# Optimization experiments

Hardware: AMD Instinct MI355X
Metric: run time of the kernel (lower is better)

## Reference

```python
import jax, jax.numpy as jnp
import numpy as np

B, N, F_IN, T = 8, 325, 32, 24
H, C = 4, 32  # num_heads, out_channels
K = 3         # k_neighbors


def _build_graph(seed=0):
    rng = np.random.default_rng(seed)
    dist = rng.uniform(0.1, 1.0, size=(N, N)).astype(np.float32)
    np.fill_diagonal(dist, 0.0)
    # per-row: k nearest among strictly-positive distances
    masked = np.where(dist > 0, dist, np.inf)
    idx = np.argsort(masked, axis=1)[:, :K]           # (N, K)
    rows = np.arange(N)[:, None]
    nd = dist[rows, idx]                              # (N, K)
    w = 1.0 / (nd + 1e-6)
    w = w / (w.sum(axis=1, keepdims=True) + 1e-6)
    adj_mask = np.zeros((N, N), np.float32)
    init_w = np.zeros((N, N), np.float32)
    adj_mask[rows, idx] = 1.0
    init_w[rows, idx] = w
    return adj_mask, init_w


def setup_inputs() -> dict:
    key = jax.random.key(0)
    k1, k2, k3, k4 = jax.random.split(key, 4)
    adj_mask, init_w = _build_graph()
    x = jax.random.normal(k1, (B, N, F_IN, T), dtype=jnp.float32)
    W_w = jax.random.normal(k2, (H * C, F_IN), dtype=jnp.float32) * (1.0 / np.sqrt(F_IN))
    W_b = jnp.zeros((H * C,), dtype=jnp.float32)
    attn_w = jax.random.normal(k3, (H, 2 * C), dtype=jnp.float32) * (1.0 / np.sqrt(2 * C))
    return {
        "x": x,
        "W_w": W_w,
        "W_b": W_b,
        "attn_w": attn_w,
        "initial_weights": jnp.asarray(init_w),
        "initial_weights_base": jnp.asarray(init_w),
        "adj_mask": jnp.asarray(adj_mask),
    }


def _constrain(w, base, adj_mask):
    w = jnp.clip(w, base * 0.5, base * 1.5)
    w = jnp.maximum(w, 0.0)
    s = jnp.sum(w * adj_mask, axis=1, keepdims=True)
    s = s + (s == 0).astype(w.dtype) * 1e-6
    return w * adj_mask / s


def reference(x, W_w, W_b, attn_w, initial_weights, initial_weights_base, adj_mask):
    b, n, f_in, t = x.shape
    xp = jnp.transpose(x, (0, 3, 1, 2))                    # (B,T,N,F)
    Wh = (xp @ W_w.T + W_b).reshape(b, t, n, H, C)         # (B,T,N,H,C)
    w = _constrain(initial_weights, initial_weights_base, adj_mask)
    a1, a2 = attn_w[:, :C], attn_w[:, C:]
    # attn(cat[Wh_i, Wh_j]) == Wh_i.a1 + Wh_j.a2 (no bias)
    f1 = jnp.einsum('btnhc,hc->btnh', Wh, a1)
    f2 = jnp.einsum('btnhc,hc->btnh', Wh, a2)
    e = f1[:, :, :, None, :] + f2[:, :, None, :, :]        # (B,T,N,N,H)
    score = jax.nn.leaky_relu(e, negative_slope=0.2)
    score = score * adj_mask[None, None, :, :, None] + w[None, None, :, :, None]
    attention = jax.nn.softmax(score, axis=3)              # softmax over j (includes zeroed non-edges, as in torch)
    out = jnp.einsum('btijh,btjhc->btihc', attention, Wh).reshape(b, t, n, H * C)
    return jnp.transpose(out, (0, 2, 3, 1))                # (B,N,H*C,T)
```

## Files before the change

kernel.cpp:

```cpp
#include <hip/hip_runtime.h>
#include <math.h>

#define Bq 8
#define Nq 325
#define F_INq 32
#define Tq 24
#define HCq 128
#define KMAX 4

__global__ __launch_bounds__(192) void prep_kernel(
    const float* __restrict__ iw, const float* __restrict__ ib,
    const float* __restrict__ adj, const float* __restrict__ Ww,
    const float* __restrict__ Wb, const float* __restrict__ attnw,
    const float* __restrict__ x,
    int* __restrict__ nbr_cnt, int* __restrict__ nbr_idx, float* __restrict__ nbr_w,
    float* __restrict__ Wx, float* __restrict__ WxT, float* __restrict__ Wp,
    float* __restrict__ bx, float* __restrict__ xp) {
  int blk = blockIdx.x;
  int tid = threadIdx.x;
  if (blk < Nq) {
    if (tid >= 64) return;
    int lane = tid;
    int i = blk;
    const float* iwr = iw + (size_t)i * Nq;
    const float* ibr = ib + (size_t)i * Nq;
    const float* ar  = adj + (size_t)i * Nq;
    float wa_c[6], a_c[6];
    float sum = 0.f;
    #pragma unroll
    for (int c = 0; c < 6; ++c) {
      int j = c * 64 + lane;
      float wa = 0.f, a = 0.f;
      if (j < Nq) {
        float basev = ibr[j];
        float w = iwr[j];
        w = fminf(fmaxf(w, basev * 0.5f), basev * 1.5f);
        w = fmaxf(w, 0.f);
        a = ar[j];
        wa = w * a;
      }
      wa_c[c] = wa; a_c[c] = a;
      sum += wa;
    }
    #pragma unroll
    for (int off = 32; off >= 1; off >>= 1) sum += __shfl_xor(sum, off, 64);
    if (sum == 0.f) sum = 1e-6f;
    float inv = 1.f / sum;
    unsigned long long below = (1ull << lane) - 1ull;
    int base = 0;
    #pragma unroll
    for (int c = 0; c < 6; ++c) {
      int j = c * 64 + lane;
      bool pred = (j < Nq) && (a_c[c] != 0.f);
      unsigned long long m = __ballot(pred);
      int rank = base + __popcll(m & below);
      if (pred && rank < KMAX) {
        nbr_idx[i * KMAX + rank] = j;
        nbr_w[i * KMAX + rank]   = wa_c[c] * inv;
      }
      base += __popcll(m);
    }
    if (lane == 0) {
      int cnt = base < KMAX ? base : KMAX;
      for (int k = cnt; k < KMAX; ++k) { nbr_idx[i * KMAX + k] = 0; nbr_w[i * KMAX + k] = 0.f; }
      nbr_cnt[i] = cnt;
    }
    return;
  }
  if (blk == Nq) {
    for (int o = tid; o < HCq * F_INq; o += 192) Wx[o] = Ww[o];
    for (int o = tid; o < F_INq * HCq; o += 192) {
      int f = o >> 7, r = o & 127;
      WxT[o] = Ww[r * F_INq + f];
    }
    for (int o = tid; o < 8 * F_INq; o += 192) {
      int p = o >> 5, f = o & 31;
      int h = p & 3, c0 = (p < 4) ? 0 : 32;
      float v = 0.f;
      for (int c = 0; c < 32; ++c)
        v += Ww[(h * 32 + c) * F_INq + f] * attnw[h * 64 + c0 + c];
      Wp[o] = v;
    }
    for (int r = tid; r < 136; r += 192) {
      float v;
      if (r < HCq) {
        v = Wb[r];
      } else {
        int h = (r - HCq) & 3, c0 = (r < 132) ? 0 : 32;
        v = 0.f;
        for (int c = 0; c < 32; ++c) v += Wb[h * 32 + c] * attnw[h * 64 + c0 + c];
      }
      bx[r] = v;
    }
    return;
  }
  {
    int pblk = blk - (Nq + 1);
    int b = pblk / 13, c = pblk - b * 13;
    const float4* src = (const float4*)x + ((size_t)b * Nq + c * 25) * 192;
    float4 a = {0.f, 0.f, 0.f, 0.f};
    #pragma unroll 5
    for (int n = 0; n < 25; ++n) {
      float4 v = src[(size_t)n * 192 + tid];
      a.x += v.x; a.y += v.y; a.z += v.z; a.w += v.w;
    }
    ((float4*)xp)[(size_t)pblk * 192 + tid] = a;
  }
}

__global__ __launch_bounds__(192) void sgemm_kernel(
    const float* __restrict__ xp, const float* __restrict__ Wx,
    const float* __restrict__ bx, float* __restrict__ S) {
  __shared__ __align__(16) float sxl[768];
  int b = blockIdx.x, tid = threadIdx.x;
  float4 a = {0.f, 0.f, 0.f, 0.f};
  #pragma unroll
  for (int c = 0; c < 13; ++c) {
    float4 v = ((const float4*)xp)[(size_t)(b * 13 + c) * 192 + tid];
    a.x += v.x; a.y += v.y; a.z += v.z; a.w += v.w;
  }
  ((float4*)sxl)[tid] = a;
  __syncthreads();
  int rg = tid / 24, t = tid % 24;
  float xv[32];
  #pragma unroll
  for (int f = 0; f < 32; ++f) xv[f] = sxl[f * 24 + t];
  float* op = S + b * (HCq * Tq) + rg * 16 * Tq + t;
  #pragma unroll 2
  for (int r = rg * 16; r < rg * 16 + 16; ++r) {
    const float* wr = Wx + r * 32;
    float a0 = 325.f * bx[r], a1 = 0.f, a2 = 0.f, a3 = 0.f;
    #pragma unroll
    for (int f = 0; f < 32; f += 4) {
      a0 += wr[f]     * xv[f];
      a1 += wr[f + 1] * xv[f + 1];
      a2 += wr[f + 2] * xv[f + 2];
      a3 += wr[f + 3] * xv[f + 3];
    }
    *op = (a0 + a1) + (a2 + a3);
    op += Tq;
  }
}

__global__ __launch_bounds__(256) void fused_kernel(
    const float* __restrict__ x, const float* __restrict__ Wp,
    const float* __restrict__ WxT, const float* __restrict__ bx,
    const float* __restrict__ S,
    const int* __restrict__ nbr_cnt, const int* __restrict__ nbr_idx,
    const float* __restrict__ nbr_w, float* __restrict__ out) {
  __shared__ __align__(16) float sx[2 * 4 * 768];
  __shared__ __align__(16) float spd[2][3][96];
  __shared__ float sbp[2][96], sps[2][96];
  __shared__ float ssw[2][3];
  __shared__ int ssi[2][3], scnt2[2];
  int tid = threadIdx.x;
  int bi0 = blockIdx.x * 2;
  if (tid < 2) {
    int c = nbr_cnt[(bi0 + tid) % Nq];
    scnt2[tid] = c < 3 ? c : 3;
  }
  if (tid < 6) {
    int ii = tid / 3, k = tid - ii * 3;
    int i = (bi0 + ii) % Nq;
    ssi[ii][k] = nbr_idx[i * KMAX + k];
    ssw[ii][k] = nbr_w[i * KMAX + k];
  }
  __syncthreads();
  const float4* x4 = (const float4*)x;
  float4* sx4 = (float4*)sx;
  #pragma unroll
  for (int j = 0; j < 6; ++j) {
    int idx = tid + j * 256;
    int slot = idx / 192, e4 = idx - slot * 192;
    int ii = slot >> 2, sl = slot & 3;
    int b = (bi0 + ii) / Nq;
    int node = (sl == 0) ? ((bi0 + ii) % Nq) : ssi[ii][sl - 1];
    sx4[idx] = x4[((size_t)(b * Nq + node)) * 192 + e4];
  }
  __syncthreads();
  if (tid < 192) {
    int ii = tid / 96, r96 = tid - ii * 96;
    int h = r96 / 24, t = r96 - h * 24;
    const float* xi  = sx + (ii * 4 + 0) * 768 + t;
    const float* xj0 = sx + (ii * 4 + 1) * 768 + t;
    const float* xj1 = sx + (ii * 4 + 2) * 768 + t;
    const float* xj2 = sx + (ii * 4 + 3) * 768 + t;
    const float* w1 = Wp + h * 32;
    const float* w2 = Wp + (4 + h) * 32;
    float f1 = bx[128 + h], g0 = bx[132 + h], g1 = g0, g2 = g0;
    #pragma unroll
    for (int f = 0; f < 32; ++f) {
      float wa = w1[f], wb2 = w2[f];
      f1 += wa * xi[f * 24];
      g0 += wb2 * xj0[f * 24];
      g1 += wb2 * xj1[f * 24];
      g2 += wb2 * xj2[f * 24];
    }
    int cnt = scnt2[ii];
    float fv[3] = {g0, g1, g2};
    float sv[3];
    float m = 0.f;
    #pragma unroll
    for (int k = 0; k < 3; ++k) {
      float s = 0.f;
      if (k < cnt) {
        float e = f1 + fv[k];
        e = e > 0.f ? e : 0.2f * e;
        s = e + ssw[ii][k];
        m = fmaxf(m, s);
      }
      sv[k] = s;
    }
    float em = __expf(-m);
    float Z = (float)(Nq - cnt) * em;
    float pk[3];
    #pragma unroll
    for (int k = 0; k < 3; ++k) {
      float p = 0.f;
      if (k < cnt) { p = __expf(sv[k] - m); Z += p; }
      pk[k] = p;
    }
    float invZ = 1.f / Z;
    float bp = em * invZ;
    float ps = 0.f;
    sbp[ii][r96] = bp;
    #pragma unroll
    for (int k = 0; k < 3; ++k) {
      float pd = (k < cnt) ? pk[k] * invZ - bp : 0.f;
      spd[ii][k][r96] = pd;
      ps += pd;
    }
    sps[ii][r96] = ps;
  }
  __syncthreads();
  int lane = tid & 63;
  int w = __builtin_amdgcn_readfirstlane(tid >> 6);
  int ii = lane / 24, t = lane - ii * 24;
  bool act = (lane < 48);
  float acc[32];
  if (act) {
    int b = (bi0 + ii) / Nq;
    int ht = w * 24 + t;
    float bpv = sbp[ii][ht];
    float psv = sps[ii][ht];
    float p0 = spd[ii][0][ht], p1 = spd[ii][1][ht], p2 = spd[ii][2][ht];
    const float* Sp  = S + b * 3072 + (w * 32) * 24 + t;
    const float* bxp = bx + w * 32;
    #pragma unroll
    for (int r = 0; r < 32; ++r) acc[r] = bpv * Sp[r * 24] + psv * bxp[r];
    const float* xj0 = sx + (ii * 4 + 1) * 768 + t;
    const float* xj1 = sx + (ii * 4 + 2) * 768 + t;
    const float* xj2 = sx + (ii * 4 + 3) * 768 + t;
    const float* wtp = WxT + w * 32;
    #pragma unroll 4
    for (int f = 0; f < 32; ++f) {
      float yv = p0 * xj0[f * 24] + p1 * xj1[f * 24] + p2 * xj2[f * 24];
      const float* wr = wtp + f * 128;
      #pragma unroll
      for (int r = 0; r < 32; ++r) acc[r] += wr[r] * yv;
    }
  }
  __syncthreads();
  if (act) {
    float* otp = sx + ii * 3072 + (w * 32) * 24 + t;
    #pragma unroll
    for (int r = 0; r < 32; ++r) otp[r * 24] = acc[r];
  }
  __syncthreads();
  float4* o4 = (float4*)(out + (size_t)bi0 * 3072);
  #pragma unroll
  for (int j = 0; j < 6; ++j) {
    int idx = tid + j * 256;
    o4[idx] = sx4[idx];
  }
}

extern "C" void kernel_launch(void* const* d_in, const int* in_sizes, int n_in,
                              void* d_out, int out_size, void* d_ws, size_t ws_size,
                              hipStream_t stream) {
  const float* x     = (const float*)d_in[0];
  const float* Ww    = (const float*)d_in[1];
  const float* Wb    = (const float*)d_in[2];
  const float* attnw = (const float*)d_in[3];
  const float* iw    = (const float*)d_in[4];
  const float* ib    = (const float*)d_in[5];
  const float* adj   = (const float*)d_in[6];
  float* out = (float*)d_out;

  float* ws = (float*)d_ws;
  float* xp  = ws;
  float* S   = xp + (size_t)Bq * 13 * 768;
  float* Wx  = S + (size_t)Bq * HCq * Tq;
  float* WxT = Wx + HCq * F_INq;
  float* Wp  = WxT + F_INq * HCq;
  float* bx  = Wp + 8 * F_INq;
  int* nbr_cnt = (int*)(bx + 136);
  int* nbr_idx = nbr_cnt + Nq;
  float* nbr_w = (float*)(nbr_idx + Nq * KMAX);

  prep_kernel<<<Nq + 1 + Bq * 13, 192, 0, stream>>>(
      iw, ib, adj, Ww, Wb, attnw, x,
      nbr_cnt, nbr_idx, nbr_w, Wx, WxT, Wp, bx, xp);
  sgemm_kernel<<<Bq, 192, 0, stream>>>(xp, Wx, bx, S);
  fused_kernel<<<(Bq * Nq) / 2, 256, 0, stream>>>(x, Wp, WxT, bx, S,
                                                  nbr_cnt, nbr_idx, nbr_w, out);
}
```

Baseline: 112.9 us.

## Fold per-batch node-sum projection into fused kernel, drop sgemm launch

Removes the separate sgemm kernel that projected the per-batch node-summed features through W. The fused kernel now reduces the 13 partial sums itself into shared memory and folds the summed x into the per-f combination before the shared W multiply, using linearity. This saves one launch and a serial dependency. In exchange, every block redoes the 13-way partial reduction and the adds per f. Blocks are regrouped per batch (163 blocks per batch), which needs guards for the odd node count.

```diff
diff --git a/kernel.cpp b/kernel.cpp
--- a/kernel.cpp
+++ b/kernel.cpp
@@ -14,7 +14,7 @@
     const float* __restrict__ Wb, const float* __restrict__ attnw,
     const float* __restrict__ x,
     int* __restrict__ nbr_cnt, int* __restrict__ nbr_idx, float* __restrict__ nbr_w,
-    float* __restrict__ Wx, float* __restrict__ WxT, float* __restrict__ Wp,
+    float* __restrict__ WxT, float* __restrict__ Wp,
     float* __restrict__ bx, float* __restrict__ xp) {
   int blk = blockIdx.x;
   int tid = threadIdx.x;
@@ -68,7 +68,6 @@
     return;
   }
   if (blk == Nq) {
-    for (int o = tid; o < HCq * F_INq; o += 192) Wx[o] = Ww[o];
     for (int o = tid; o < F_INq * HCq; o += 192) {
       int f = o >> 7, r = o & 127;
       WxT[o] = Ww[r * F_INq + f];
@@ -108,60 +107,31 @@
   }
 }
 
-__global__ __launch_bounds__(192) void sgemm_kernel(
-    const float* __restrict__ xp, const float* __restrict__ Wx,
-    const float* __restrict__ bx, float* __restrict__ S) {
-  __shared__ __align__(16) float sxl[768];
-  int b = blockIdx.x, tid = threadIdx.x;
-  float4 a = {0.f, 0.f, 0.f, 0.f};
-  #pragma unroll
-  for (int c = 0; c < 13; ++c) {
-    float4 v = ((const float4*)xp)[(size_t)(b * 13 + c) * 192 + tid];
-    a.x += v.x; a.y += v.y; a.z += v.z; a.w += v.w;
-  }
-  ((float4*)sxl)[tid] = a;
-  __syncthreads();
-  int rg = tid / 24, t = tid % 24;
-  float xv[32];
-  #pragma unroll
-  for (int f = 0; f < 32; ++f) xv[f] = sxl[f * 24 + t];
-  float* op = S + b * (HCq * Tq) + rg * 16 * Tq + t;
-  #pragma unroll 2
-  for (int r = rg * 16; r < rg * 16 + 16; ++r) {
-    const float* wr = Wx + r * 32;
-    float a0 = 325.f * bx[r], a1 = 0.f, a2 = 0.f, a3 = 0.f;
-    #pragma unroll
-    for (int f = 0; f < 32; f += 4) {
-      a0 += wr[f]     * xv[f];
-      a1 += wr[f + 1] * xv[f + 1];
-      a2 += wr[f + 2] * xv[f + 2];
-      a3 += wr[f + 3] * xv[f + 3];
-    }
-    *op = (a0 + a1) + (a2 + a3);
-    op += Tq;
-  }
-}
-
 __global__ __launch_bounds__(256) void fused_kernel(
     const float* __restrict__ x, const float* __restrict__ Wp,
     const float* __restrict__ WxT, const float* __restrict__ bx,
-    const float* __restrict__ S,
+    const float* __restrict__ xp,
     const int* __restrict__ nbr_cnt, const int* __restrict__ nbr_idx,
     const float* __restrict__ nbr_w, float* __restrict__ out) {
-  __shared__ __align__(16) float sx[2 * 4 * 768];
+  __shared__ __align__(16) float sx[6144];
+  __shared__ __align__(16) float sxs[768];
   __shared__ __align__(16) float spd[2][3][96];
   __shared__ float sbp[2][96], sps[2][96];
   __shared__ float ssw[2][3];
   __shared__ int ssi[2][3], scnt2[2];
   int tid = threadIdx.x;
-  int bi0 = blockIdx.x * 2;
+  int blk = blockIdx.x;
+  int b = blk / 163;
+  int i0 = (blk - b * 163) * 2;
+  int valid1 = (i0 + 1 < Nq) ? 1 : 0;
   if (tid < 2) {
-    int c = nbr_cnt[(bi0 + tid) % Nq];
+    int i = i0 + (tid & valid1);
+    int c = nbr_cnt[i];
     scnt2[tid] = c < 3 ? c : 3;
   }
   if (tid < 6) {
     int ii = tid / 3, k = tid - ii * 3;
-    int i = (bi0 + ii) % Nq;
+    int i = i0 + (ii & valid1);
     ssi[ii][k] = nbr_idx[i * KMAX + k];
     ssw[ii][k] = nbr_w[i * KMAX + k];
   }
@@ -173,9 +143,18 @@
     int idx = tid + j * 256;
     int slot = idx / 192, e4 = idx - slot * 192;
     int ii = slot >> 2, sl = slot & 3;
-    int b = (bi0 + ii) / Nq;
-    int node = (sl == 0) ? ((bi0 + ii) % Nq) : ssi[ii][sl - 1];
+    int node = (sl == 0) ? (i0 + (ii & valid1)) : ssi[ii][sl - 1];
     sx4[idx] = x4[((size_t)(b * Nq + node)) * 192 + e4];
+  }
+  if (tid < 192) {
+    const float4* xpb = (const float4*)xp + (size_t)b * 13 * 192;
+    float4 a = {0.f, 0.f, 0.f, 0.f};
+    #pragma unroll
+    for (int c = 0; c < 13; ++c) {
+      float4 v = xpb[c * 192 + tid];
+      a.x += v.x; a.y += v.y; a.z += v.z; a.w += v.w;
+    }
+    ((float4*)sxs)[tid] = a;
   }
   __syncthreads();
   if (tid < 192) {
@@ -239,22 +218,23 @@
   bool act = (lane < 48);
   float acc[32];
   if (act) {
-    int b = (bi0 + ii) / Nq;
     int ht = w * 24 + t;
     float bpv = sbp[ii][ht];
     float psv = sps[ii][ht];
     float p0 = spd[ii][0][ht], p1 = spd[ii][1][ht], p2 = spd[ii][2][ht];
-    const float* Sp  = S + b * 3072 + (w * 32) * 24 + t;
+    float initc = psv + 325.f * bpv;
     const float* bxp = bx + w * 32;
     #pragma unroll
-    for (int r = 0; r < 32; ++r) acc[r] = bpv * Sp[r * 24] + psv * bxp[r];
+    for (int r = 0; r < 32; ++r) acc[r] = initc * bxp[r];
     const float* xj0 = sx + (ii * 4 + 1) * 768 + t;
     const float* xj1 = sx + (ii * 4 + 2) * 768 + t;
     const float* xj2 = sx + (ii * 4 + 3) * 768 + t;
+    const float* xsp = sxs + t;
     const float* wtp = WxT + w * 32;
     #pragma unroll 4
     for (int f = 0; f < 32; ++f) {
-      float yv = p0 * xj0[f * 24] + p1 * xj1[f * 24] + p2 * xj2[f * 24];
+      float yv = p0 * xj0[f * 24] + p1 * xj1[f * 24] + p2 * xj2[f * 24]
+               + bpv * xsp[f * 24];
       const float* wr = wtp + f * 128;
       #pragma unroll
       for (int r = 0; r < 32; ++r) acc[r] += wr[r] * yv;
@@ -267,11 +247,12 @@
     for (int r = 0; r < 32; ++r) otp[r * 24] = acc[r];
   }
   __syncthreads();
-  float4* o4 = (float4*)(out + (size_t)bi0 * 3072);
+  float4* o4 = (float4*)(out + ((size_t)(b * Nq + i0)) * 3072);
+  int lim = valid1 ? 1536 : 768;
   #pragma unroll
   for (int j = 0; j < 6; ++j) {
     int idx = tid + j * 256;
-    o4[idx] = sx4[idx];
+    if (idx < lim) o4[idx] = sx4[idx];
   }
 }
 
@@ -289,9 +270,7 @@
 
   float* ws = (float*)d_ws;
   float* xp  = ws;
-  float* S   = xp + (size_t)Bq * 13 * 768;
-  float* Wx  = S + (size_t)Bq * HCq * Tq;
-  float* WxT = Wx + HCq * F_INq;
+  float* WxT = xp + (size_t)Bq * 13 * 768;
   float* Wp  = WxT + F_INq * HCq;
   float* bx  = Wp + 8 * F_INq;
   int* nbr_cnt = (int*)(bx + 136);
@@ -300,8 +279,7 @@
 
   prep_kernel<<<Nq + 1 + Bq * 13, 192, 0, stream>>>(
       iw, ib, adj, Ww, Wb, attnw, x,
-      nbr_cnt, nbr_idx, nbr_w, Wx, WxT, Wp, bx, xp);
-  sgemm_kernel<<<Bq, 192, 0, stream>>>(xp, Wx, bx, S);
-  fused_kernel<<<(Bq * Nq) / 2, 256, 0, stream>>>(x, Wp, WxT, bx, S,
-                                                  nbr_cnt, nbr_idx, nbr_w, out);
+      nbr_cnt, nbr_idx, nbr_w, WxT, Wp, bx, xp);
+  fused_kernel<<<Bq * 163, 256, 0, stream>>>(x, Wp, WxT, bx, xp,
+                                             nbr_cnt, nbr_idx, nbr_w, out);
 }
```

After: 104.7 us. 1.08x faster.
